# Optimization experiments

Hardware: AMD Instinct MI355X
Metric: run time of the kernel (lower is better)

Reference implementation:

```python
import jax, jax.numpy as jnp
import numpy as np

B, C, H, W, O, K = 4, 64, 128, 128, 64, 3


def setup_inputs() -> dict:
    key = jax.random.key(0)
    kx, ko, kw = jax.random.split(key, 3)
    x = jax.random.normal(kx, (B, C, H, W), dtype=jnp.float32)
    offset = jax.random.normal(ko, (B, 2 * K * K, H, W), dtype=jnp.float32)
    stdv = 1.0 / np.sqrt(C * K * K)
    weight = jax.random.uniform(kw, (O, C, K, K), dtype=jnp.float32,
                                minval=-stdv, maxval=stdv)
    return {"x": x, "offset": offset, "weight": weight}


def _deform_conv(x, offset, weight):
    b, c, h, w = x.shape
    o = weight.shape[0]
    k = weight.shape[2]
    kk = k * k
    # kernel tap displacements, flattened row-major (ki*K + kj), centered at 0
    taps = jnp.arange(k) - k // 2
    di = jnp.repeat(taps, k)            # [kk]
    dj = jnp.tile(taps, k)              # [kk]
    # base sampling coords: base_i[h,1,kk], base_j[1,w,kk]
    base_i = (jnp.arange(h)[:, None, None] + di).astype(jnp.float32)
    base_j = (jnp.arange(w)[None, :, None] + dj).astype(jnp.float32)
    # offset: [b, kk, 2, h, w] -> [b, h, w, kk, 2]
    off = offset.reshape(b, kk, 2, h, w).transpose(0, 3, 4, 1, 2)
    ci = off[..., 0] + base_i           # [b,h,w,kk] float sample row coords
    cj = off[..., 1] + base_j           # [b,h,w,kk] float sample col coords

    i_lt = jnp.floor(ci).astype(jnp.int32)
    i_rb = jnp.ceil(ci).astype(jnp.int32)
    j_lt = jnp.floor(cj).astype(jnp.int32)
    j_rb = jnp.ceil(cj).astype(jnp.int32)

    def gather(ii, jj):
        # out-of-bounds samples contribute 0 (matching the torch masking)
        inb = (ii >= 0) & (ii < h) & (jj >= 0) & (jj < w)
        ic = jnp.clip(ii, 0, h - 1)
        jc = jnp.clip(jj, 0, w - 1)
        # per-image gather: xb[:, i, j] with i,j of shape [h,w,kk] -> [c,h,w,kk]
        v = jax.vmap(lambda xb, i, j: xb[:, i, j])(x, ic, jc)  # [b,c,h,w,kk]
        return v * inb[:, None].astype(x.dtype)

    vals_lt = gather(i_lt, j_lt)
    vals_rb = gather(i_rb, j_rb)
    vals_rt = gather(i_lt, j_rb)
    vals_lb = gather(i_rb, j_lt)

    # fractional parts (gradient flows to offset only through these)
    fi = (ci - i_lt.astype(ci.dtype))[:, None]   # [b,1,h,w,kk]
    fj = (cj - j_lt.astype(cj.dtype))[:, None]

    vals_t = vals_lt + fj * (vals_rt - vals_lt)
    vals_b = vals_lb + fj * (vals_rb - vals_lb)
    mapped = vals_t + fi * (vals_b - vals_t)     # [b,c,h,w,kk]

    # final GEMM: weight [o, c*kk] x im2col-like [c*kk, b*h*w]
    return jnp.einsum('ock,bchwk->bohw', weight.reshape(o, c, kk), mapped)


def reference(x, offset, weight):
    return _deform_conv(x, offset, weight)
```

## Files before the change

### kernel.cpp

```cpp
#include <hip/hip_runtime.h>

namespace {
constexpr int B = 4, C = 64, H = 128, W = 128, O = 64, KK = 9;
constexpr int PREPT = 256;
constexpr int MAINT = 512;
constexpr int WF_ELEMS = KK * 2 * 4 * 64 * 8;
constexpr size_t XT_BYTES = (size_t)B * H * W * C * 2;
constexpr size_t WF_BYTES = (size_t)WF_ELEMS * 2;
constexpr size_t WS_NEED  = XT_BYTES + WF_BYTES;
}

typedef float    f32x4 __attribute__((ext_vector_type(4)));
typedef _Float16 f16x2 __attribute__((ext_vector_type(2)));
typedef _Float16 f16x8 __attribute__((ext_vector_type(8)));

__device__ __forceinline__ unsigned hpack2(float a, float b) {
  f16x2 v; v[0] = (_Float16)a; v[1] = (_Float16)b;
  return __builtin_bit_cast(unsigned, v);
}
__device__ __forceinline__ void gload16(const void* g, void* l) {
  __builtin_amdgcn_global_load_lds(
      (const __attribute__((address_space(1))) unsigned*)g,
      (__attribute__((address_space(3))) unsigned*)l, 16, 0, 0);
}

__global__ __launch_bounds__(PREPT)
void prep_fused(const float* __restrict__ x, const float* __restrict__ wgt,
                unsigned* __restrict__ xt_u32, unsigned short* __restrict__ wf) {
  __shared__ float st[64][65];
  const int t = threadIdx.x;

  const int gid = blockIdx.x * PREPT + t;
  if (gid < WF_ELEMS) {
    const int e = gid & 7, lane = (gid >> 3) & 63, mt = (gid >> 9) & 3;
    const int ks = (gid >> 11) & 1, tap = gid >> 12;
    const int o = mt * 16 + (lane & 15);
    const int c = ks * 32 + ((lane >> 4) << 3) + e;
    const _Float16 hv = (_Float16)wgt[(size_t)o * (C * KK) + c * KK + tap];
    wf[gid] = __builtin_bit_cast(unsigned short, hv);
  }

  const int half = blockIdx.x & 1, h = (blockIdx.x >> 1) & 127, b = blockIdx.x >> 8;
  const int w0 = half * 64;
#pragma unroll
  for (int it = 0; it < 4; ++it) {
    const int w4 = (t & 15) * 4, c = it * 16 + (t >> 4);
    const float4 v = *(const float4*)&x[((size_t)(b * C + c) * H + h) * W + w0 + w4];
    st[w4 + 0][c] = v.x; st[w4 + 1][c] = v.y;
    st[w4 + 2][c] = v.z; st[w4 + 3][c] = v.w;
  }
  __syncthreads();
#pragma unroll
  for (int it = 0; it < 8; ++it) {
    const int idx = it * PREPT + t;
    const int w = idx >> 5, c2 = (idx & 31) * 2;
    xt_u32[(size_t)(((b * H + h) * W) + w0 + w) * 32 + (c2 >> 1)] = hpack2(st[w][c2], st[w][c2 + 1]);
  }
}

__global__ __launch_bounds__(MAINT) __attribute__((amdgpu_waves_per_eu(6)))
void deform_mfma(const float* __restrict__ offs, const char* __restrict__ xt,
                 const char* __restrict__ wfg, float* __restrict__ out) {
  __shared__ unsigned short s_wf[2][4096];
  __shared__ unsigned short s_m[128 * 64];
  __shared__ unsigned s_pw[8][KK][16][2];
  __shared__ unsigned s_pp[8][KK][16];

  const int t = threadIdx.x, l = t & 63, wid = t >> 6;
  const int nid = (blockIdx.x & 7) * 64 + (blockIdx.x >> 3);
  const int h = nid & 127, b = nid >> 7;
  const int wbase = wid * 16;

#pragma unroll
  for (int it = 0; it < 3; ++it) {
    const int item = it * 64 + l;
    if (item < KK * 16) {
      const int tap = item >> 4, pix = item & 15;
      const int ki = tap / 3, kj = tap - ki * 3;
      const int w = wbase + pix;
      const float* ob = offs + ((size_t)b * (2 * KK) + 2 * tap) * (H * W) + h * W + w;
      const float oi = ob[0], oj = ob[H * W];
      const float ci = oi + (float)(h + ki - 1);
      const float cj = oj + (float)(w + kj - 1);
      const float fli = floorf(ci), flj = floorf(cj);
      const int i0 = (int)fli, j0 = (int)flj, i1 = i0 + 1, j1 = j0 + 1;
      const float fi = ci - fli, fj = cj - flj, gi = 1.f - fi, gj = 1.f - fj;
      const bool bi0 = (unsigned)i0 < (unsigned)H, bi1 = (unsigned)i1 < (unsigned)H;
      const bool bj0 = (unsigned)j0 < (unsigned)W, bj1 = (unsigned)j1 < (unsigned)W;
      const int ic0 = min(max(i0, 0), H - 1), ic1 = min(max(i1, 0), H - 1);
      const int jc0 = min(max(j0, 0), W - 1), jc1 = min(max(j1, 0), W - 1);
      const float w00 = gi * gj * (float)(bi0 && bj0);
      const float w01 = gi * fj * (float)(bi0 && bj1);
      const float w10 = fi * gj * (float)(bi1 && bj0);
      const float w11 = fi * fj * (float)(bi1 && bj1);
      s_pw[wid][tap][pix][0] = hpack2(w00, w01);
      s_pw[wid][tap][pix][1] = hpack2(w10, w11);
      s_pp[wid][tap][pix] = (unsigned)jc0 | ((unsigned)ic0 << 7) |
                            ((unsigned)jc1 << 14) | ((unsigned)ic1 << 21);
    }
  }

  const int pix8 = l >> 3, oct = l & 7, cb = oct << 4;
  const char* xb = xt + ((size_t)b * H * W << 7) + cb;

  char* smb = (char*)s_m;
  char* smw = (char*)s_wf;
  const int wb  = ((wid * 16 + pix8) << 7) + ((oct ^ pix8) << 4);
  const int rr  = wid * 16 + (l & 15);
  const int rd0 = (rr << 7) + ((((l >> 4)    ) ^ (l & 7)) << 4);
  const int rd1 = (rr << 7) + (((4 + (l >> 4)) ^ (l & 7)) << 4);

  f32x4 acc[4];
#pragma unroll
  for (int mt = 0; mt < 4; ++mt) acc[mt] = (f32x4)0.f;

  uint4 g[2][4];
#define ISSUE(TAPX, HS) do {                                                   \
    const unsigned v_ = s_pp[wid][(TAPX)][(HS) * 8 + pix8];                    \
    const unsigned i0s = v_ & 0x3F80u;                                         \
    const unsigned j0_ = v_ & 0x7Fu;                                           \
    const unsigned j1_ = (v_ >> 14) & 0x7Fu;                                   \
    const unsigned i1s = (v_ >> 14) & 0x3F80u;                                 \
    g[HS][0] = *(const uint4*)(xb + ((size_t)(i0s | j0_) << 7));               \
    g[HS][1] = *(const uint4*)(xb + ((size_t)(i0s | j1_) << 7));               \
    g[HS][2] = *(const uint4*)(xb + ((size_t)(i1s | j0_) << 7));               \
    g[HS][3] = *(const uint4*)(xb + ((size_t)(i1s | j1_) << 7));               \
  } while (0)

#define LERPH(c0_, c1_, c2_, c3_) __builtin_bit_cast(unsigned, (f16x2)(        \
    __builtin_bit_cast(f16x2, c0_) * W00 + __builtin_bit_cast(f16x2, c1_) * W01 + \
    __builtin_bit_cast(f16x2, c2_) * W10 + __builtin_bit_cast(f16x2, c3_) * W11))

#define STAGE(TAPV, HS) do {                                                   \
    const uint2 pk = *(const uint2*)&s_pw[wid][(TAPV)][(HS) * 8 + pix8][0];    \
    const f16x2 pa_ = __builtin_bit_cast(f16x2, pk.x);                         \
    const f16x2 pb_ = __builtin_bit_cast(f16x2, pk.y);                         \
    const f16x2 W00 = {pa_[0], pa_[0]}, W01 = {pa_[1], pa_[1]};                \
    const f16x2 W10 = {pb_[0], pb_[0]}, W11 = {pb_[1], pb_[1]};                \
    uint4* gc = g[HS];                                                         \
    uint4 r;                                                                   \
    r.x = LERPH(gc[0].x, gc[1].x, gc[2].x, gc[3].x);                           \
    r.y = LERPH(gc[0].y, gc[1].y, gc[2].y, gc[3].y);                           \
    r.z = LERPH(gc[0].z, gc[1].z, gc[2].z, gc[3].z);                           \
    r.w = LERPH(gc[0].w, gc[1].w, gc[2].w, gc[3].w);                           \
    *(uint4*)(smb + wb + (HS) * 1024) = r;                                     \
  } while (0)

  gload16(wfg + (size_t)t * 16, smw + t * 16);
  ISSUE(0, 0);
  ISSUE(0, 1);

#pragma unroll 1
  for (int tap = 0; tap < KK; ++tap) {
    __syncthreads();

    if (tap + 1 < KK)
      gload16(wfg + (size_t)(tap + 1) * 8192 + t * 16,
              smw + ((tap + 1) & 1) * 8192 + t * 16);

    STAGE(tap, 0);
    if (tap + 1 < KK) ISSUE(tap + 1, 0);
    STAGE(tap, 1);
    if (tap + 1 < KK) ISSUE(tap + 1, 1);

    const char* wl = smw + (tap & 1) * 8192;
    const f16x8 b0 = *(const f16x8*)(smb + rd0);
    const f16x8 b1 = *(const f16x8*)(smb + rd1);
    __builtin_amdgcn_s_setprio(1);
#pragma unroll
    for (int mt = 0; mt < 4; ++mt) {
      const f16x8 a0 = *(const f16x8*)(wl + mt * 1024 + l * 16);
      acc[mt] = __builtin_amdgcn_mfma_f32_16x16x32_f16(a0, b0, acc[mt], 0, 0, 0);
    }
#pragma unroll
    for (int mt = 0; mt < 4; ++mt) {
      const f16x8 a1 = *(const f16x8*)(wl + 4096 + mt * 1024 + l * 16);
      acc[mt] = __builtin_amdgcn_mfma_f32_16x16x32_f16(a1, b1, acc[mt], 0, 0, 0);
    }
    __builtin_amdgcn_s_setprio(0);
  }
#undef ISSUE
#undef LERPH
#undef STAGE

#pragma unroll
  for (int mt = 0; mt < 4; ++mt)
#pragma unroll
    for (int j = 0; j < 4; ++j) {
      const int o = mt * 16 + ((l >> 4) << 2) + j;
      out[((size_t)(b * O + o) * H + h) * W + wbase + (l & 15)] = acc[mt][j];
    }
}

namespace fb {
constexpr int WT = 32, CH = 16, NCHUNK = 4, KC = 144, WPAD = 68;
}
__global__ __launch_bounds__(PREPT, 2)
void deform_conv_fused(const float* __restrict__ x, const float* __restrict__ offs,
                       const float* __restrict__ wgt, float* __restrict__ out) {
  using namespace fb;
  __shared__ int   s_i0[KK][WT];
  __shared__ int   s_j0[KK][WT];
  __shared__ float s_fi[KK][WT];
  __shared__ float s_fj[KK][WT];
  __shared__ float s_w[KC][WPAD];
  __shared__ float s_m[KC][WT + 1];
  const int t = threadIdx.x;
  const int nwt = W / WT;
  const int wt = blockIdx.x % nwt, h = (blockIdx.x / nwt) % H, b = blockIdx.x / (nwt * H);
  const int w0 = wt * WT;
  for (int idx = t; idx < KK * WT; idx += PREPT) {
    const int k = idx / WT, p = idx % WT, w = w0 + p;
    const float oi = offs[(((size_t)b * (2 * KK) + 2 * k) * H + h) * W + w];
    const float oj = offs[(((size_t)b * (2 * KK) + 2 * k + 1) * H + h) * W + w];
    const float ci = oi + (float)(h + (k / 3) - 1), cj = oj + (float)(w + (k % 3) - 1);
    const float fli = floorf(ci), flj = floorf(cj);
    s_i0[k][p] = (int)fli; s_j0[k][p] = (int)flj;
    s_fi[k][p] = ci - fli; s_fj[k][p] = cj - flj;
  }
  float acc[8];
#pragma unroll
  for (int i = 0; i < 8; ++i) acc[i] = 0.f;
  const int p = t & (WT - 1), ob = (t >> 5) * 8;
  for (int cc = 0; cc < NCHUNK; ++cc) {
    const int c0 = cc * CH;
    __syncthreads();
    for (int idx = t; idx < O * KC; idx += PREPT)
      s_w[idx % KC][idx / KC] = wgt[(size_t)(idx / KC) * (C * KK) + (size_t)c0 * KK + idx % KC];
    for (int idx = t; idx < CH * KK * WT; idx += PREPT) {
      const int pp = idx & (WT - 1), rest = idx >> 5, k = rest % KK, cl = rest / KK;
      const int i0 = s_i0[k][pp], j0 = s_j0[k][pp], i1 = i0 + 1, j1 = j0 + 1;
      const float fi = s_fi[k][pp], fj = s_fj[k][pp];
      const float* xb = x + (size_t)(b * C + c0 + cl) * H * W;
      const float v00 = ((unsigned)i0 < (unsigned)H && (unsigned)j0 < (unsigned)W) ? xb[i0 * W + j0] : 0.f;
      const float v01 = ((unsigned)i0 < (unsigned)H && (unsigned)j1 < (unsigned)W) ? xb[i0 * W + j1] : 0.f;
      const float v10 = ((unsigned)i1 < (unsigned)H && (unsigned)j0 < (unsigned)W) ? xb[i1 * W + j0] : 0.f;
      const float v11 = ((unsigned)i1 < (unsigned)H && (unsigned)j1 < (unsigned)W) ? xb[i1 * W + j1] : 0.f;
      const float top = v00 + fj * (v01 - v00), bot = v10 + fj * (v11 - v10);
      s_m[cl * KK + k][pp] = top + fi * (bot - top);
    }
    __syncthreads();
#pragma unroll 4
    for (int k = 0; k < KC; ++k) {
      const float a = s_m[k][p];
      const float4 wv0 = *reinterpret_cast<const float4*>(&s_w[k][ob]);
      const float4 wv1 = *reinterpret_cast<const float4*>(&s_w[k][ob + 4]);
      acc[0] += a * wv0.x; acc[1] += a * wv0.y; acc[2] += a * wv0.z; acc[3] += a * wv0.w;
      acc[4] += a * wv1.x; acc[5] += a * wv1.y; acc[6] += a * wv1.z; acc[7] += a * wv1.w;
    }
  }
#pragma unroll
  for (int i = 0; i < 8; ++i)
    out[(((size_t)b * O + ob + i) * H + h) * W + w0 + p] = acc[i];
}

extern "C" void kernel_launch(void* const* d_in, const int* in_sizes, int n_in,
                              void* d_out, int out_size, void* d_ws, size_t ws_size,
                              hipStream_t stream) {
  const float* x    = (const float*)d_in[0];
  const float* offs = (const float*)d_in[1];
  const float* wgt  = (const float*)d_in[2];
  float* out = (float*)d_out;

  if (ws_size < WS_NEED) {
    deform_conv_fused<<<B * H * (W / 32), PREPT, 0, stream>>>(x, offs, wgt, out);
    return;
  }
  char* xt = (char*)d_ws;
  unsigned short* wf = (unsigned short*)(xt + XT_BYTES);

  prep_fused<<<B * H * 2, PREPT, 0, stream>>>(x, wgt, (unsigned*)xt, wf);
  deform_mfma<<<B * H, MAINT, 0, stream>>>(offs, xt, (const char*)wf, out);
}
```

Before: 30.38 us.

## Switch main kernel to 32x32x16 MFMA with 4 waves covering 32 pixels each

The main deformable-conv kernel moves from 512 threads of 16x16x32 MFMAs to 256 threads, where each wave owns 32 output pixels and uses 32x32x16 f16 MFMAs. The weight prep layout is reordered to match the new A-operand fragment layout, and each wave gathers and interpolates four 8-pixel groups per tap instead of two. The aim is fewer, larger MFMA instructions and fewer LDS fragment reads per FLOP. In exchange, each thread holds more gathered data in registers and fewer waves are resident, which may hide gather latency less well.

```diff
diff --git a/kernel.cpp b/kernel.cpp
--- a/kernel.cpp
+++ b/kernel.cpp
@@ -3,16 +3,16 @@
 namespace {
 constexpr int B = 4, C = 64, H = 128, W = 128, O = 64, KK = 9;
 constexpr int PREPT = 256;
-constexpr int MAINT = 512;
-constexpr int WF_ELEMS = KK * 2 * 4 * 64 * 8;
+constexpr int MAINT = 256;
+constexpr int WF_ELEMS = KK * 4096;
 constexpr size_t XT_BYTES = (size_t)B * H * W * C * 2;
 constexpr size_t WF_BYTES = (size_t)WF_ELEMS * 2;
 constexpr size_t WS_NEED  = XT_BYTES + WF_BYTES;
 }
 
-typedef float    f32x4 __attribute__((ext_vector_type(4)));
-typedef _Float16 f16x2 __attribute__((ext_vector_type(2)));
-typedef _Float16 f16x8 __attribute__((ext_vector_type(8)));
+typedef float    f32x16 __attribute__((ext_vector_type(16)));
+typedef _Float16 f16x2  __attribute__((ext_vector_type(2)));
+typedef _Float16 f16x8  __attribute__((ext_vector_type(8)));
 
 __device__ __forceinline__ unsigned hpack2(float a, float b) {
   f16x2 v; v[0] = (_Float16)a; v[1] = (_Float16)b;
@@ -32,10 +32,10 @@
 
   const int gid = blockIdx.x * PREPT + t;
   if (gid < WF_ELEMS) {
-    const int e = gid & 7, lane = (gid >> 3) & 63, mt = (gid >> 9) & 3;
-    const int ks = (gid >> 11) & 1, tap = gid >> 12;
-    const int o = mt * 16 + (lane & 15);
-    const int c = ks * 32 + ((lane >> 4) << 3) + e;
+    const int e = gid & 7, lane = (gid >> 3) & 63;
+    const int mt = (gid >> 9) & 1, ks = (gid >> 10) & 3, tap = gid >> 12;
+    const int o = mt * 32 + (lane & 31);
+    const int c = ks * 16 + ((lane >> 5) << 3) + e;
     const _Float16 hv = (_Float16)wgt[(size_t)o * (C * KK) + c * KK + tap];
     wf[gid] = __builtin_bit_cast(unsigned short, hv);
   }
@@ -58,24 +58,24 @@
   }
 }
 
-__global__ __launch_bounds__(MAINT) __attribute__((amdgpu_waves_per_eu(6)))
+__global__ __launch_bounds__(MAINT) __attribute__((amdgpu_waves_per_eu(3)))
 void deform_mfma(const float* __restrict__ offs, const char* __restrict__ xt,
                  const char* __restrict__ wfg, float* __restrict__ out) {
   __shared__ unsigned short s_wf[2][4096];
   __shared__ unsigned short s_m[128 * 64];
-  __shared__ unsigned s_pw[8][KK][16][2];
-  __shared__ unsigned s_pp[8][KK][16];
+  __shared__ unsigned s_pw[4][KK][32][2];
+  __shared__ unsigned s_pp[4][KK][32];
 
   const int t = threadIdx.x, l = t & 63, wid = t >> 6;
   const int nid = (blockIdx.x & 7) * 64 + (blockIdx.x >> 3);
   const int h = nid & 127, b = nid >> 7;
-  const int wbase = wid * 16;
-
-#pragma unroll
-  for (int it = 0; it < 3; ++it) {
+  const int wbase = wid * 32;
+
+#pragma unroll
+  for (int it = 0; it < 5; ++it) {
     const int item = it * 64 + l;
-    if (item < KK * 16) {
-      const int tap = item >> 4, pix = item & 15;
+    if (item < KK * 32) {
+      const int tap = item >> 5, pix = item & 31;
       const int ki = tap / 3, kj = tap - ki * 3;
       const int w = wbase + pix;
       const float* ob = offs + ((size_t)b * (2 * KK) + 2 * tap) * (H * W) + h * W + w;
@@ -105,16 +105,14 @@
 
   char* smb = (char*)s_m;
   char* smw = (char*)s_wf;
-  const int wb  = ((wid * 16 + pix8) << 7) + ((oct ^ pix8) << 4);
-  const int rr  = wid * 16 + (l & 15);
-  const int rd0 = (rr << 7) + ((((l >> 4)    ) ^ (l & 7)) << 4);
-  const int rd1 = (rr << 7) + (((4 + (l >> 4)) ^ (l & 7)) << 4);
-
-  f32x4 acc[4];
-#pragma unroll
-  for (int mt = 0; mt < 4; ++mt) acc[mt] = (f32x4)0.f;
-
-  uint4 g[2][4];
+  const int wb0 = ((wid * 32 + pix8) << 7) + ((oct ^ pix8) << 4);
+  const int rdb = (wid * 32 + (l & 31)) << 7;
+
+  f32x16 acc[2];
+  acc[0] = (f32x16)0.f;
+  acc[1] = (f32x16)0.f;
+
+  uint4 g[4][4];
 #define ISSUE(TAPX, HS) do {                                                   \
     const unsigned v_ = s_pp[wid][(TAPX)][(HS) * 8 + pix8];                    \
     const unsigned i0s = v_ & 0x3F80u;                                         \
@@ -143,39 +141,42 @@
     r.y = LERPH(gc[0].y, gc[1].y, gc[2].y, gc[3].y);                           \
     r.z = LERPH(gc[0].z, gc[1].z, gc[2].z, gc[3].z);                           \
     r.w = LERPH(gc[0].w, gc[1].w, gc[2].w, gc[3].w);                           \
-    *(uint4*)(smb + wb + (HS) * 1024) = r;                                     \
+    *(uint4*)(smb + wb0 + (HS) * 1024) = r;                                    \
   } while (0)
 
   gload16(wfg + (size_t)t * 16, smw + t * 16);
-  ISSUE(0, 0);
-  ISSUE(0, 1);
+  gload16(wfg + 4096 + (size_t)t * 16, smw + 4096 + t * 16);
+  ISSUE(0, 0); ISSUE(0, 1); ISSUE(0, 2); ISSUE(0, 3);
 
 #pragma unroll 1
   for (int tap = 0; tap < KK; ++tap) {
     __syncthreads();
 
-    if (tap + 1 < KK)
-      gload16(wfg + (size_t)(tap + 1) * 8192 + t * 16,
-              smw + ((tap + 1) & 1) * 8192 + t * 16);
+    if (tap + 1 < KK) {
+      const char* src = wfg + (size_t)(tap + 1) * 8192 + t * 16;
+      char* dst = smw + ((tap + 1) & 1) * 8192 + t * 16;
+      gload16(src, dst);
+      gload16(src + 4096, dst + 4096);
+    }
 
     STAGE(tap, 0);
     if (tap + 1 < KK) ISSUE(tap + 1, 0);
     STAGE(tap, 1);
     if (tap + 1 < KK) ISSUE(tap + 1, 1);
+    STAGE(tap, 2);
+    if (tap + 1 < KK) ISSUE(tap + 1, 2);
+    STAGE(tap, 3);
+    if (tap + 1 < KK) ISSUE(tap + 1, 3);
 
     const char* wl = smw + (tap & 1) * 8192;
-    const f16x8 b0 = *(const f16x8*)(smb + rd0);
-    const f16x8 b1 = *(const f16x8*)(smb + rd1);
     __builtin_amdgcn_s_setprio(1);
 #pragma unroll
-    for (int mt = 0; mt < 4; ++mt) {
-      const f16x8 a0 = *(const f16x8*)(wl + mt * 1024 + l * 16);
-      acc[mt] = __builtin_amdgcn_mfma_f32_16x16x32_f16(a0, b0, acc[mt], 0, 0, 0);
-    }
-#pragma unroll
-    for (int mt = 0; mt < 4; ++mt) {
-      const f16x8 a1 = *(const f16x8*)(wl + 4096 + mt * 1024 + l * 16);
-      acc[mt] = __builtin_amdgcn_mfma_f32_16x16x32_f16(a1, b1, acc[mt], 0, 0, 0);
+    for (int ks = 0; ks < 4; ++ks) {
+      const f16x8 bf = *(const f16x8*)(smb + rdb + ((((ks << 1) + (l >> 5)) ^ (l & 7)) << 4));
+      const f16x8 a0 = *(const f16x8*)(wl + (((ks * 2 + 0) * 64 + l) << 4));
+      acc[0] = __builtin_amdgcn_mfma_f32_32x32x16_f16(a0, bf, acc[0], 0, 0, 0);
+      const f16x8 a1 = *(const f16x8*)(wl + (((ks * 2 + 1) * 64 + l) << 4));
+      acc[1] = __builtin_amdgcn_mfma_f32_32x32x16_f16(a1, bf, acc[1], 0, 0, 0);
     }
     __builtin_amdgcn_s_setprio(0);
   }
@@ -184,11 +185,11 @@
 #undef STAGE
 
 #pragma unroll
-  for (int mt = 0; mt < 4; ++mt)
-#pragma unroll
-    for (int j = 0; j < 4; ++j) {
-      const int o = mt * 16 + ((l >> 4) << 2) + j;
-      out[((size_t)(b * O + o) * H + h) * W + wbase + (l & 15)] = acc[mt][j];
+  for (int mt = 0; mt < 2; ++mt)
+#pragma unroll
+    for (int r = 0; r < 16; ++r) {
+      const int o = mt * 32 + (r & 3) + 8 * (r >> 2) + 4 * (l >> 5);
+      out[((size_t)(b * O + o) * H + h) * W + wbase + (l & 31)] = acc[mt][r];
     }
 }
 
```

After: 32.12 us. 5.7% more time.

## Keep all weight taps resident in LDS with 1024-thread two-row blocks

Applied to the files above, without the earlier changes.

Adds a main kernel that loads the full fp16 weight tensor (all 9 taps) into dynamic LDS once per block and processes two image rows with 16 waves, removing the per-tap weight double-buffer refill and the per-tap __syncthreads. The tap loop is fully unrolled. The old 512-thread kernel is kept as a fallback if setting the dynamic LDS limit fails. The cost is about 150KB of LDS per block, which allows only one block per CU, plus a host-side attribute call on every launch. Each wave also still writes its own staging slice, so the per-tap barrier is dropped without cross-wave dependence.

```diff
diff --git a/kernel.cpp b/kernel.cpp
--- a/kernel.cpp
+++ b/kernel.cpp
@@ -3,11 +3,11 @@
 namespace {
 constexpr int B = 4, C = 64, H = 128, W = 128, O = 64, KK = 9;
 constexpr int PREPT = 256;
-constexpr int MAINT = 512;
 constexpr int WF_ELEMS = KK * 2 * 4 * 64 * 8;
+constexpr int WF_BYTES_I = WF_ELEMS * 2;
 constexpr size_t XT_BYTES = (size_t)B * H * W * C * 2;
-constexpr size_t WF_BYTES = (size_t)WF_ELEMS * 2;
-constexpr size_t WS_NEED  = XT_BYTES + WF_BYTES;
+constexpr size_t WS_NEED  = XT_BYTES + (size_t)WF_BYTES_I;
+constexpr int DYN_LDS = WF_BYTES_I + 32768 + 18432 + 9216;
 }
 
 typedef float    f32x4 __attribute__((ext_vector_type(4)));
@@ -58,65 +58,38 @@
   }
 }
 
-__global__ __launch_bounds__(MAINT) __attribute__((amdgpu_waves_per_eu(6)))
-void deform_mfma(const float* __restrict__ offs, const char* __restrict__ xt,
-                 const char* __restrict__ wfg, float* __restrict__ out) {
-  __shared__ unsigned short s_wf[2][4096];
-  __shared__ unsigned short s_m[128 * 64];
-  __shared__ unsigned s_pw[8][KK][16][2];
-  __shared__ unsigned s_pp[8][KK][16];
-
-  const int t = threadIdx.x, l = t & 63, wid = t >> 6;
-  const int nid = (blockIdx.x & 7) * 64 + (blockIdx.x >> 3);
-  const int h = nid & 127, b = nid >> 7;
-  const int wbase = wid * 16;
-
-#pragma unroll
-  for (int it = 0; it < 3; ++it) {
-    const int item = it * 64 + l;
-    if (item < KK * 16) {
-      const int tap = item >> 4, pix = item & 15;
-      const int ki = tap / 3, kj = tap - ki * 3;
-      const int w = wbase + pix;
-      const float* ob = offs + ((size_t)b * (2 * KK) + 2 * tap) * (H * W) + h * W + w;
-      const float oi = ob[0], oj = ob[H * W];
-      const float ci = oi + (float)(h + ki - 1);
-      const float cj = oj + (float)(w + kj - 1);
-      const float fli = floorf(ci), flj = floorf(cj);
-      const int i0 = (int)fli, j0 = (int)flj, i1 = i0 + 1, j1 = j0 + 1;
-      const float fi = ci - fli, fj = cj - flj, gi = 1.f - fi, gj = 1.f - fj;
-      const bool bi0 = (unsigned)i0 < (unsigned)H, bi1 = (unsigned)i1 < (unsigned)H;
-      const bool bj0 = (unsigned)j0 < (unsigned)W, bj1 = (unsigned)j1 < (unsigned)W;
-      const int ic0 = min(max(i0, 0), H - 1), ic1 = min(max(i1, 0), H - 1);
-      const int jc0 = min(max(j0, 0), W - 1), jc1 = min(max(j1, 0), W - 1);
-      const float w00 = gi * gj * (float)(bi0 && bj0);
-      const float w01 = gi * fj * (float)(bi0 && bj1);
-      const float w10 = fi * gj * (float)(bi1 && bj0);
-      const float w11 = fi * fj * (float)(bi1 && bj1);
-      s_pw[wid][tap][pix][0] = hpack2(w00, w01);
-      s_pw[wid][tap][pix][1] = hpack2(w10, w11);
-      s_pp[wid][tap][pix] = (unsigned)jc0 | ((unsigned)ic0 << 7) |
-                            ((unsigned)jc1 << 14) | ((unsigned)ic1 << 21);
-    }
-  }
-
-  const int pix8 = l >> 3, oct = l & 7, cb = oct << 4;
-  const char* xb = xt + ((size_t)b * H * W << 7) + cb;
-
-  char* smb = (char*)s_m;
-  char* smw = (char*)s_wf;
-  const int wb  = ((wid * 16 + pix8) << 7) + ((oct ^ pix8) << 4);
-  const int rr  = wid * 16 + (l & 15);
-  const int rd0 = (rr << 7) + ((((l >> 4)    ) ^ (l & 7)) << 4);
-  const int rd1 = (rr << 7) + (((4 + (l >> 4)) ^ (l & 7)) << 4);
-
-  f32x4 acc[4];
-#pragma unroll
-  for (int mt = 0; mt < 4; ++mt) acc[mt] = (f32x4)0.f;
-
-  uint4 g[2][4];
-#define ISSUE(TAPX, HS) do {                                                   \
-    const unsigned v_ = s_pp[wid][(TAPX)][(HS) * 8 + pix8];                    \
+#define PARAMS_BODY(NW, SPW, SPP)                                              \
+  _Pragma("unroll")                                                            \
+  for (int it = 0; it < 3; ++it) {                                             \
+    const int item = it * 64 + l;                                              \
+    if (item < KK * 16) {                                                      \
+      const int tap = item >> 4, pix = item & 15;                              \
+      const int ki = tap / 3, kj = tap - ki * 3;                               \
+      const int w = wbase + pix;                                               \
+      const float* ob = offs + ((size_t)b * (2 * KK) + 2 * tap) * (H * W) + h * W + w; \
+      const float oi = ob[0], oj = ob[H * W];                                  \
+      const float ci = oi + (float)(h + ki - 1);                               \
+      const float cj = oj + (float)(w + kj - 1);                               \
+      const float fli = floorf(ci), flj = floorf(cj);                          \
+      const int i0 = (int)fli, j0 = (int)flj, i1 = i0 + 1, j1 = j0 + 1;        \
+      const float fi = ci - fli, fj = cj - flj, gi = 1.f - fi, gj = 1.f - fj;  \
+      const bool bi0 = (unsigned)i0 < (unsigned)H, bi1 = (unsigned)i1 < (unsigned)H; \
+      const bool bj0 = (unsigned)j0 < (unsigned)W, bj1 = (unsigned)j1 < (unsigned)W; \
+      const int ic0 = min(max(i0, 0), H - 1), ic1 = min(max(i1, 0), H - 1);    \
+      const int jc0 = min(max(j0, 0), W - 1), jc1 = min(max(j1, 0), W - 1);    \
+      const float w00 = gi * gj * (float)(bi0 && bj0);                         \
+      const float w01 = gi * fj * (float)(bi0 && bj1);                         \
+      const float w10 = fi * gj * (float)(bi1 && bj0);                         \
+      const float w11 = fi * fj * (float)(bi1 && bj1);                         \
+      SPW(tap, pix, 0) = hpack2(w00, w01);                                     \
+      SPW(tap, pix, 1) = hpack2(w10, w11);                                     \
+      SPP(tap, pix) = (unsigned)jc0 | ((unsigned)ic0 << 7) |                   \
+                      ((unsigned)jc1 << 14) | ((unsigned)ic1 << 21);           \
+    }                                                                          \
+  }
+
+#define ISSUE_BODY(SPP, TAPX, HS) do {                                         \
+    const unsigned v_ = SPP(TAPX, (HS) * 8 + pix8);                            \
     const unsigned i0s = v_ & 0x3F80u;                                         \
     const unsigned j0_ = v_ & 0x7Fu;                                           \
     const unsigned j1_ = (v_ >> 14) & 0x7Fu;                                   \
@@ -131,8 +104,8 @@
     __builtin_bit_cast(f16x2, c0_) * W00 + __builtin_bit_cast(f16x2, c1_) * W01 + \
     __builtin_bit_cast(f16x2, c2_) * W10 + __builtin_bit_cast(f16x2, c3_) * W11))
 
-#define STAGE(TAPV, HS) do {                                                   \
-    const uint2 pk = *(const uint2*)&s_pw[wid][(TAPV)][(HS) * 8 + pix8][0];    \
+#define STAGE_BODY(SPW, TAPV, HS) do {                                         \
+    const uint2 pk = *(const uint2*)&SPW(TAPV, (HS) * 8 + pix8, 0);            \
     const f16x2 pa_ = __builtin_bit_cast(f16x2, pk.x);                         \
     const f16x2 pb_ = __builtin_bit_cast(f16x2, pk.y);                         \
     const f16x2 W00 = {pa_[0], pa_[0]}, W01 = {pa_[1], pa_[1]};                \
@@ -146,22 +119,130 @@
     *(uint4*)(smb + wb + (HS) * 1024) = r;                                     \
   } while (0)
 
+__global__ __launch_bounds__(1024) __attribute__((amdgpu_waves_per_eu(4)))
+void deform_mfma_res(const float* __restrict__ offs, const char* __restrict__ xt,
+                     const char* __restrict__ wfg, float* __restrict__ out) {
+  extern __shared__ char dyn[];
+  char* wlds = dyn;
+  char* smb  = dyn + WF_BYTES_I;
+  unsigned* pwp = (unsigned*)(dyn + WF_BYTES_I + 32768);
+  unsigned* ppp = (unsigned*)(dyn + WF_BYTES_I + 32768 + 18432);
+
+#define SPWr(tap, pix, j) pwp[(((wid * KK + (tap)) * 16 + (pix)) << 1) + (j)]
+#define SPPr(tap, pix)    ppp[(wid * KK + (tap)) * 16 + (pix)]
+
+  const int t = threadIdx.x, l = t & 63, wid = t >> 6;
+  const int nid = (blockIdx.x & 7) * 32 + (blockIdx.x >> 3);
+  const int b = nid >> 6, rp = nid & 63;
+  const int h = rp * 2 + (wid >> 3);
+  const int wbase = (wid & 7) * 16;
+
+  for (int off = t * 16; off < WF_BYTES_I; off += 16384)
+    gload16(wfg + off, wlds + off);
+
+  PARAMS_BODY(16, SPWr, SPPr)
+
+  const int pix8 = l >> 3, oct = l & 7, cb = oct << 4;
+  const char* xb = xt + ((size_t)b * H * W << 7) + cb;
+
+  const int wb  = ((wid * 16 + pix8) << 7) + ((oct ^ pix8) << 4);
+  const int rr  = wid * 16 + (l & 15);
+  const int rd0 = (rr << 7) + ((((l >> 4)    ) ^ (l & 7)) << 4);
+  const int rd1 = (rr << 7) + (((4 + (l >> 4)) ^ (l & 7)) << 4);
+
+  f32x4 acc[4];
+#pragma unroll
+  for (int mt = 0; mt < 4; ++mt) acc[mt] = (f32x4)0.f;
+
+  uint4 g[2][4];
+  ISSUE_BODY(SPPr, 0, 0);
+  ISSUE_BODY(SPPr, 0, 1);
+
+  __syncthreads();
+
+#pragma unroll
+  for (int tap = 0; tap < KK; ++tap) {
+    STAGE_BODY(SPWr, tap, 0);
+    if (tap + 1 < KK) ISSUE_BODY(SPPr, tap + 1, 0);
+    STAGE_BODY(SPWr, tap, 1);
+    if (tap + 1 < KK) ISSUE_BODY(SPPr, tap + 1, 1);
+
+    const char* wl = wlds + tap * 8192;
+    const f16x8 b0 = *(const f16x8*)(smb + rd0);
+    const f16x8 b1 = *(const f16x8*)(smb + rd1);
+    __builtin_amdgcn_s_setprio(1);
+#pragma unroll
+    for (int mt = 0; mt < 4; ++mt) {
+      const f16x8 a0 = *(const f16x8*)(wl + mt * 1024 + l * 16);
+      acc[mt] = __builtin_amdgcn_mfma_f32_16x16x32_f16(a0, b0, acc[mt], 0, 0, 0);
+    }
+#pragma unroll
+    for (int mt = 0; mt < 4; ++mt) {
+      const f16x8 a1 = *(const f16x8*)(wl + 4096 + mt * 1024 + l * 16);
+      acc[mt] = __builtin_amdgcn_mfma_f32_16x16x32_f16(a1, b1, acc[mt], 0, 0, 0);
+    }
+    __builtin_amdgcn_s_setprio(0);
+  }
+
+#pragma unroll
+  for (int mt = 0; mt < 4; ++mt)
+#pragma unroll
+    for (int j = 0; j < 4; ++j) {
+      const int o = mt * 16 + ((l >> 4) << 2) + j;
+      out[((size_t)(b * O + o) * H + h) * W + wbase + (l & 15)] = acc[mt][j];
+    }
+#undef SPWr
+#undef SPPr
+}
+
+__global__ __launch_bounds__(512) __attribute__((amdgpu_waves_per_eu(6)))
+void deform_mfma_static(const float* __restrict__ offs, const char* __restrict__ xt,
+                        const char* __restrict__ wfg, float* __restrict__ out) {
+  __shared__ unsigned short s_wf[2][4096];
+  __shared__ unsigned short s_m[128 * 64];
+  __shared__ unsigned s_pw[8][KK][16][2];
+  __shared__ unsigned s_pp[8][KK][16];
+
+#define SPWs(tap, pix, j) s_pw[wid][tap][pix][j]
+#define SPPs(tap, pix)    s_pp[wid][tap][pix]
+
+  const int t = threadIdx.x, l = t & 63, wid = t >> 6;
+  const int nid = (blockIdx.x & 7) * 64 + (blockIdx.x >> 3);
+  const int h = nid & 127, b = nid >> 7;
+  const int wbase = wid * 16;
+
+  PARAMS_BODY(8, SPWs, SPPs)
+
+  const int pix8 = l >> 3, oct = l & 7, cb = oct << 4;
+  const char* xb = xt + ((size_t)b * H * W << 7) + cb;
+
+  char* smb = (char*)s_m;
+  char* smw = (char*)s_wf;
+  const int wb  = ((wid * 16 + pix8) << 7) + ((oct ^ pix8) << 4);
+  const int rr  = wid * 16 + (l & 15);
+  const int rd0 = (rr << 7) + ((((l >> 4)    ) ^ (l & 7)) << 4);
+  const int rd1 = (rr << 7) + (((4 + (l >> 4)) ^ (l & 7)) << 4);
+
+  f32x4 acc[4];
+#pragma unroll
+  for (int mt = 0; mt < 4; ++mt) acc[mt] = (f32x4)0.f;
+
+  uint4 g[2][4];
   gload16(wfg + (size_t)t * 16, smw + t * 16);
-  ISSUE(0, 0);
-  ISSUE(0, 1);
+  ISSUE_BODY(SPPs, 0, 0);
+  ISSUE_BODY(SPPs, 0, 1);
 
 #pragma unroll 1
   for (int tap = 0; tap < KK; ++tap) {
     __syncthreads();
-
     if (tap + 1 < KK)
       gload16(wfg + (size_t)(tap + 1) * 8192 + t * 16,
               smw + ((tap + 1) & 1) * 8192 + t * 16);
 
-    STAGE(tap, 0);
-    if (tap + 1 < KK) ISSUE(tap + 1, 0);
-    STAGE(tap, 1);
-    if (tap + 1 < KK) ISSUE(tap + 1, 1);
+    STAGE_BODY(SPWs, tap, 0);
+    if (tap + 1 < KK) ISSUE_BODY(SPPs, tap + 1, 0);
+    STAGE_BODY(SPWs, tap, 1);
+    if (tap + 1 < KK) ISSUE_BODY(SPPs, tap + 1, 1);
 
     const char* wl = smw + (tap & 1) * 8192;
     const f16x8 b0 = *(const f16x8*)(smb + rd0);
@@ -179,9 +260,6 @@
     }
     __builtin_amdgcn_s_setprio(0);
   }
-#undef ISSUE
-#undef LERPH
-#undef STAGE
 
 #pragma unroll
   for (int mt = 0; mt < 4; ++mt)
@@ -190,6 +268,8 @@
       const int o = mt * 16 + ((l >> 4) << 2) + j;
       out[((size_t)(b * O + o) * H + h) * W + wbase + (l & 15)] = acc[mt][j];
     }
+#undef SPWs
+#undef SPPs
 }
 
 namespace fb {
@@ -270,5 +350,12 @@
   unsigned short* wf = (unsigned short*)(xt + XT_BYTES);
 
   prep_fused<<<B * H * 2, PREPT, 0, stream>>>(x, wgt, (unsigned*)xt, wf);
-  deform_mfma<<<B * H, MAINT, 0, stream>>>(offs, xt, (const char*)wf, out);
-}
+
+  hipError_t e = hipFuncSetAttribute((const void*)deform_mfma_res,
+                                     hipFuncAttributeMaxDynamicSharedMemorySize,
+                                     DYN_LDS);
+  if (e == hipSuccess)
+    deform_mfma_res<<<B * H / 2, 1024, DYN_LDS, stream>>>(offs, xt, (const char*)wf, out);
+  else
+    deform_mfma_static<<<B * H, 512, 0, stream>>>(offs, xt, (const char*)wf, out);
+}
```

Result: faster. 28.95 us (median of 2 runs) (-4.7%).
